# Kernel optimization log

Hardware: AMD Instinct MI355X
Metric: run time of the kernel (lower is better)

The kernel has to match this reference:

```python
import jax, jax.numpy as jnp
import numpy as np

N = 500_000      # num nodes
E = 8_000_000    # num edges (before self-loops)
F_IN, H, C = 16, 8, 2


def setup_inputs() -> dict:
    key = jax.random.key(0)
    k = jax.random.split(key, 6)
    x = jax.random.normal(k[0], (N, F_IN), dtype=jnp.float32)
    edge_index = jax.random.randint(k[1], (2, E), 0, N, dtype=jnp.int32)
    # Glorot-style init like PyG GCNConv
    W1 = jax.random.normal(k[2], (F_IN, H), dtype=jnp.float32) * (1.0 / np.sqrt(F_IN))
    b1 = jnp.zeros((H,), dtype=jnp.float32)
    W2 = jax.random.normal(k[3], (H, C), dtype=jnp.float32) * (1.0 / np.sqrt(H))
    b2 = jnp.zeros((C,), dtype=jnp.float32)
    return {"x": x, "W1": W1, "b1": b1, "W2": W2, "b2": b2, "edge_index": edge_index}


def reference(x, W1, b1, W2, b2, edge_index):
    # GCNConv: out = D^{-1/2} (A + I) D^{-1/2} X W + b   (PyG semantics)
    row, col = edge_index[0], edge_index[1]           # messages flow row -> col
    loop = jnp.arange(N, dtype=row.dtype)
    row = jnp.concatenate([row, loop])                # add self-loops
    col = jnp.concatenate([col, loop])
    deg = jax.ops.segment_sum(jnp.ones_like(col, dtype=x.dtype), col, num_segments=N)
    dinv = jnp.where(deg > 0, jax.lax.rsqrt(deg), jnp.zeros_like(deg))
    norm = dinv[row] * dinv[col]                      # [E+N]

    def propagate(h):  # h: [N, d] -> normalized scatter-add aggregation
        msg = h[row] * norm[:, None]                  # gather + scale, [E+N, d]
        return jax.ops.segment_sum(msg, col, num_segments=N)

    h = jax.nn.relu(propagate(x @ W1) + b1)           # [N, 8]
    out = propagate(h @ W2) + b2                      # [N, 2]
    return jax.nn.log_softmax(out, axis=1)
```

## Files before the change

kernel.cpp:

```cpp
#include <hip/hip_runtime.h>

#define TPB 256
#define NBLK_EDGE 512
#define CHUNKE 16384
#define BIN_SHIFT 9
#define BIN_SIZE 512
#define MAXK 1024
#define ROW_BITS 19
#define ROW_MASK ((1u << ROW_BITS) - 1)
#define Q_SHIFT 17
#define NKEY 2048
#define CAP 12288

typedef _Float16 half8  __attribute__((ext_vector_type(8)));
typedef _Float16 half2v __attribute__((ext_vector_type(2)));

__device__ __forceinline__ int wave_scan_incl(int v, int lane) {
#pragma unroll
    for (int d = 1; d < 64; d <<= 1) {
        int u = __shfl_up(v, d, 64);
        if (lane >= d) v += u;
    }
    return v;
}

__device__ __forceinline__ int block_excl_scan_1024(int v, int tid, int* wsum) {
    int lane = tid & 63, wv = tid >> 6;
    int incl = wave_scan_incl(v, lane);
    if (lane == 63) wsum[wv] = incl;
    __syncthreads();
    if (tid < 16) {
        int w = wsum[tid];
#pragma unroll
        for (int d = 1; d < 16; d <<= 1) {
            int u = __shfl_up(w, d, 16);
            if (tid >= d) w += u;
        }
        wsum[tid] = w;
    }
    __syncthreads();
    return incl - v + (wv ? wsum[wv - 1] : 0);
}

__global__ void __launch_bounds__(1024) k_hist(
        const int* __restrict__ col, int E, int chunk,
        int* __restrict__ cntB, int* __restrict__ cntT) {
    __shared__ int lh[MAXK];
    int blk = blockIdx.x, tid = threadIdx.x;
    lh[tid] = 0;
    __syncthreads();
    int s = blk * chunk, e_ = min(s + chunk, E);
    for (int e = s + tid; e < e_; e += 1024)
        atomicAdd(&lh[col[e] >> BIN_SHIFT], 1);
    __syncthreads();
    int v = lh[tid];
    cntB[(size_t)blk * MAXK + tid] = v;
    cntT[(size_t)tid * NBLK_EDGE + blk] = v;
}

__global__ void k_colscan(int* __restrict__ cntT, int* __restrict__ ghist) {
    __shared__ int part[256];
    int b = blockIdx.x, tid = threadIdx.x;
    size_t base = (size_t)b * NBLK_EDGE;
    int t2 = tid * 2;
    int c0 = cntT[base + t2], c1 = cntT[base + t2 + 1];
    int sum = c0 + c1;
    part[tid] = sum;
    __syncthreads();
    for (int off = 1; off < 256; off <<= 1) {
        int v = (tid >= off) ? part[tid - off] : 0;
        __syncthreads();
        part[tid] += v;
        __syncthreads();
    }
    int excl = part[tid] - sum;
    cntT[base + t2]     = excl;
    cntT[base + t2 + 1] = excl + c0;
    if (tid == 255) ghist[b] = part[255];
}

__global__ void __launch_bounds__(1024) k_scan(
        const int* __restrict__ ghist, int K, int* __restrict__ binBase,
        int* __restrict__ scratchCur) {
    __shared__ int wsum[16];
    int tid = threadIdx.x;
    if (tid == 0) *scratchCur = 0;
    int val = (tid < K) ? ghist[tid] : 0;
    int excl = block_excl_scan_1024(val, tid, wsum);
    binBase[tid] = excl;
    if (tid == K - 1) binBase[K] = excl + val;
}

__global__ void __launch_bounds__(1024) k_reorder(
        const int* __restrict__ row, const int* __restrict__ col,
        int E, int chunk,
        const int* __restrict__ binBase, const int* __restrict__ cntB,
        const int* __restrict__ cntT, unsigned* __restrict__ packed) {
    __shared__ unsigned sorted[CHUNKE];
    __shared__ unsigned short sbin[CHUNKE];
    __shared__ int lcur[MAXK], lbase[MAXK], gbase[MAXK];
    __shared__ int wsum[16];
    int blk = blockIdx.x, tid = threadIdx.x;
    int s = blk * chunk, e_ = min(s + chunk, E), len = e_ - s;
    size_t bb = (size_t)blk * MAXK;
    int c0 = cntB[bb + tid];
    int excl = block_excl_scan_1024(c0, tid, wsum);
    lbase[tid] = excl;
    lcur[tid] = excl;
    gbase[tid] = binBase[tid] + cntT[(size_t)tid * NBLK_EDGE + blk];
    __syncthreads();
    for (int i = tid; i < len; i += blockDim.x) {
        int cc = col[s + i];
        int b = cc >> BIN_SHIFT;
        int slot = atomicAdd(&lcur[b], 1);
        sorted[slot] = ((unsigned)(cc & (BIN_SIZE - 1)) << ROW_BITS) | (unsigned)row[s + i];
        sbin[slot] = (unsigned short)b;
    }
    __syncthreads();
    for (int i = tid; i < len; i += blockDim.x) {
        int b = sbin[i];
        packed[gbase[b] + (i - lbase[b])] = sorted[i];
    }
}

__global__ void __launch_bounds__(1024) k_binsort(
        unsigned* __restrict__ packed, const int* __restrict__ binBase,
        unsigned* __restrict__ scratch, int* __restrict__ scratchCur,
        const float* __restrict__ x, const float* __restrict__ W1,
        half8* __restrict__ g0, int* __restrict__ keyptr, int N, int E, int K) {
    __shared__ unsigned buf2[CAP];
    __shared__ int cnt[NKEY], cur[NKEY];
    __shared__ float w1s[128];
    __shared__ int wsum[16];
    __shared__ int sbShared;
    int tid = threadIdx.x;
    int bin = blockIdx.x;
    int s = binBase[bin], t = binBase[bin + 1];
    int len = t - s;
    bool fast = (len <= CAP);
    cnt[tid] = 0;
    cnt[tid + 1024] = 0;
    if (tid < 128) w1s[tid] = W1[tid];
    if (!fast && tid == 0) sbShared = atomicAdd(scratchCur, len);
    __syncthreads();
    for (int i = tid; i < len; i += 1024) {
        unsigned v = packed[s + i];
        int k = (int)((v >> ROW_BITS) << 2) | (int)((v & ROW_MASK) >> Q_SHIFT);
        atomicAdd(&cnt[k], 1);
    }
    __syncthreads();
    int t2 = tid * 2;
    int c0 = cnt[t2], c1 = cnt[t2 + 1];
    int excl = block_excl_scan_1024(c0 + c1, tid, wsum);
    cur[t2] = excl;
    cur[t2 + 1] = excl + c0;
    int base = bin << BIN_SHIFT;
    if (base + (t2 >> 2) < N) keyptr[((size_t)bin << 11) + t2] = s + excl;
    if (base + ((t2 + 1) >> 2) < N) keyptr[((size_t)bin << 11) + t2 + 1] = s + excl + c0;
    float di = 0.0f;
    int node = base + tid;
    if (tid < BIN_SIZE && node < N) {
        int deg = cnt[4 * tid] + cnt[4 * tid + 1] + cnt[4 * tid + 2] + cnt[4 * tid + 3];
        di = rsqrtf((float)(deg + 1));
    }
    if (bin == K - 1 && tid == 0) keyptr[(size_t)4 * N] = E;
    __syncthreads();
    if (fast) {
        for (int i = tid; i < len; i += 1024) {
            unsigned v = packed[s + i];
            int k = (int)((v >> ROW_BITS) << 2) | (int)((v & ROW_MASK) >> Q_SHIFT);
            int slot = atomicAdd(&cur[k], 1);
            buf2[slot] = v;
        }
        __syncthreads();
        for (int i = tid; i < len; i += 1024) packed[s + i] = buf2[i];
    } else {
        unsigned* stg = scratch + sbShared;
        for (int i = tid; i < len; i += 1024) stg[i] = packed[s + i];
        __threadfence();
        __syncthreads();
        for (int i = tid; i < len; i += 1024) {
            unsigned v = stg[i];
            int k = (int)((v >> ROW_BITS) << 2) | (int)((v & ROW_MASK) >> Q_SHIFT);
            int slot = atomicAdd(&cur[k], 1);
            packed[s + slot] = v;
        }
    }
    if (tid < BIN_SIZE && node < N) {
        const float4* xv = (const float4*)(x + (size_t)node * 16);
        float h[8];
#pragma unroll
        for (int j = 0; j < 8; ++j) h[j] = 0.0f;
#pragma unroll
        for (int kk = 0; kk < 4; ++kk) {
            float4 a = xv[kk];
            int kb = kk * 4;
#pragma unroll
            for (int j = 0; j < 8; ++j)
                h[j] += a.x * w1s[kb * 8 + j] + a.y * w1s[(kb + 1) * 8 + j]
                      + a.z * w1s[(kb + 2) * 8 + j] + a.w * w1s[(kb + 3) * 8 + j];
        }
        half8 g;
#pragma unroll
        for (int j = 0; j < 8; ++j) g[j] = (_Float16)(di * h[j]);
        g0[node] = g;
    }
}

__global__ void __launch_bounds__(TPB) k_gather1(
        const unsigned* __restrict__ packed, const int* __restrict__ keyptr,
        const half8* __restrict__ g0, const float* __restrict__ b1,
        const float* __restrict__ W2, half2v* __restrict__ g1, int N) {
    int i = blockIdx.x * blockDim.x + threadIdx.x;
    bool act = (i < N);
    int kp0 = 0, kp1 = 0, kp2 = 0, kp3 = 0, kp4 = 0;
    if (act) {
        int4 k4 = ((const int4*)keyptr)[i];
        kp0 = k4.x; kp1 = k4.y; kp2 = k4.z; kp3 = k4.w;
        kp4 = keyptr[4 * i + 4];
    }
    float acc[8];
#pragma unroll
    for (int j = 0; j < 8; ++j) acc[j] = 0.0f;
#pragma unroll
    for (int q = 0; q < 4; ++q) {
        int e = (q == 0) ? kp0 : (q == 1) ? kp1 : (q == 2) ? kp2 : kp3;
        int t = (q == 0) ? kp1 : (q == 1) ? kp2 : (q == 2) ? kp3 : kp4;
        if (act) {
            for (; e + 4 <= t; e += 4) {
                unsigned p0 = packed[e], p1 = packed[e + 1],
                         p2 = packed[e + 2], p3 = packed[e + 3];
                half8 v0 = g0[p0 & ROW_MASK];
                half8 v1 = g0[p1 & ROW_MASK];
                half8 v2 = g0[p2 & ROW_MASK];
                half8 v3 = g0[p3 & ROW_MASK];
#pragma unroll
                for (int j = 0; j < 8; ++j)
                    acc[j] += (float)v0[j] + (float)v1[j] + (float)v2[j] + (float)v3[j];
            }
            for (; e < t; ++e) {
                half8 v = g0[packed[e] & ROW_MASK];
#pragma unroll
                for (int j = 0; j < 8; ++j) acc[j] += (float)v[j];
            }
        }
        __syncthreads();
    }
    if (act) {
        half8 self = g0[i];
        float di = rsqrtf((float)(kp4 - kp0 + 1));
        float o0 = 0.0f, o1 = 0.0f;
#pragma unroll
        for (int j = 0; j < 8; ++j) {
            float hj = fmaxf(di * (acc[j] + (float)self[j]) + b1[j], 0.0f);
            o0 += hj * W2[j * 2 + 0];
            o1 += hj * W2[j * 2 + 1];
        }
        half2v g;
        g.x = (_Float16)(di * o0);
        g.y = (_Float16)(di * o1);
        g1[i] = g;
    }
}

__global__ void __launch_bounds__(TPB) k_gather2(
        const unsigned* __restrict__ packed, const int* __restrict__ keyptr,
        const half2v* __restrict__ g1, const float* __restrict__ b2,
        float* __restrict__ out, int N) {
    int i = blockIdx.x * blockDim.x + threadIdx.x;
    if (i >= N) return;
    int s = keyptr[4 * i], t = keyptr[4 * i + 4];
    half2v sg = g1[i];
    float a0 = (float)sg.x, a1 = (float)sg.y;
    int e = s;
    for (; e + 4 <= t; e += 4) {
        unsigned p0 = packed[e], p1 = packed[e + 1], p2 = packed[e + 2], p3 = packed[e + 3];
        half2v v0 = g1[p0 & ROW_MASK];
        half2v v1 = g1[p1 & ROW_MASK];
        half2v v2 = g1[p2 & ROW_MASK];
        half2v v3 = g1[p3 & ROW_MASK];
        a0 += (float)v0.x + (float)v1.x + (float)v2.x + (float)v3.x;
        a1 += (float)v0.y + (float)v1.y + (float)v2.y + (float)v3.y;
    }
    for (; e < t; ++e) {
        half2v v = g1[packed[e] & ROW_MASK];
        a0 += (float)v.x;
        a1 += (float)v.y;
    }
    float di = rsqrtf((float)(t - s + 1));
    float o0 = di * a0 + b2[0];
    float o1 = di * a1 + b2[1];
    float m = fmaxf(o0, o1);
    float lse = m + logf(expf(o0 - m) + expf(o1 - m));
    ((float2*)out)[i] = make_float2(o0 - lse, o1 - lse);
}

extern "C" void kernel_launch(void* const* d_in, const int* in_sizes, int n_in,
                              void* d_out, int out_size, void* d_ws, size_t ws_size,
                              hipStream_t stream) {
    const float* x  = (const float*)d_in[0];
    const float* W1 = (const float*)d_in[1];
    const float* b1 = (const float*)d_in[2];
    const float* W2 = (const float*)d_in[3];
    const float* b2 = (const float*)d_in[4];
    const int*   ei = (const int*)d_in[5];

    const int N = in_sizes[0] / 16;
    const int E = in_sizes[5] / 2;
    const int* row = ei;
    const int* col = ei + E;
    const int K = (N + BIN_SIZE - 1) >> BIN_SHIFT;

    float* ws   = (float*)d_ws;
    half8* g0   = (half8*)ws;
    half2v* g1  = (half2v*)(ws + (size_t)4 * N);
    unsigned* scratch = (unsigned*)(ws + (size_t)5 * N);
    int* keyptr = (int*)(ws + (size_t)13 * N);
    int*   meta = (int*)(ws + (size_t)17 * N + 8);
    int* ghist      = meta;
    int* binBase    = meta + MAXK;
    int* scratchCur = meta + 2 * MAXK + 16;
    unsigned* packed = (unsigned*)(meta + 3 * MAXK);
    int* cntB = (int*)(packed + E);
    int* cntT = cntB + (size_t)MAXK * NBLK_EDGE;

    float* out = (float*)d_out;

    const int gN = (N + TPB - 1) / TPB;
    const int chunk = (E + NBLK_EDGE - 1) / NBLK_EDGE;

    k_hist   <<<NBLK_EDGE, 1024, 0, stream>>>(col, E, chunk, cntB, cntT);
    k_colscan<<<K, 256, 0, stream>>>(cntT, ghist);
    k_scan   <<<1, MAXK, 0, stream>>>(ghist, K, binBase, scratchCur);
    k_reorder<<<NBLK_EDGE, 1024, 0, stream>>>(row, col, E, chunk,
                                              binBase, cntB, cntT, packed);
    k_binsort<<<K, 1024, 0, stream>>>(packed, binBase, scratch, scratchCur,
                                      x, W1, g0, keyptr, N, E, K);
    k_gather1<<<gN, TPB, 0, stream>>>(packed, keyptr, g0, b1, W2, g1, N);
    k_gather2<<<gN, TPB, 0, stream>>>(packed, keyptr, g1, b2, out, N);
}
```

Measured before the change: 351.2 us.

## Use 16-lane groups per node in gathers and drop quadrant subkey sort

The two gather kernels now assign a 16-lane group to each destination node, striding over its edges and reducing with xor shuffles, instead of one thread walking every edge of a node. The bin sort now keys only on the destination column, dropping the row-quadrant subkey, so keyptr shrinks to N+1 offsets and the workspace layout is compacted. The intent is to remove load imbalance and serial edge loops in the gathers and to make the packed index reads coalesced. The trade-off is losing the row-ordered locality the quadrant subsort gave within each node's edge list, and most lanes sit idle once a node has fewer than 16 edges.

```diff
diff --git a/kernel.cpp b/kernel.cpp
--- a/kernel.cpp
+++ b/kernel.cpp
@@ -8,9 +8,8 @@
 #define MAXK 1024
 #define ROW_BITS 19
 #define ROW_MASK ((1u << ROW_BITS) - 1)
-#define Q_SHIFT 17
-#define NKEY 2048
 #define CAP 12288
+#define GV_TPB 512
 
 typedef _Float16 half8  __attribute__((ext_vector_type(8)));
 typedef _Float16 half2v __attribute__((ext_vector_type(2)));
@@ -129,7 +128,7 @@
         const float* __restrict__ x, const float* __restrict__ W1,
         half8* __restrict__ g0, int* __restrict__ keyptr, int N, int E, int K) {
     __shared__ unsigned buf2[CAP];
-    __shared__ int cnt[NKEY], cur[NKEY];
+    __shared__ int cnt[BIN_SIZE], cur[BIN_SIZE];
     __shared__ float w1s[128];
     __shared__ int wsum[16];
     __shared__ int sbShared;
@@ -138,38 +137,31 @@
     int s = binBase[bin], t = binBase[bin + 1];
     int len = t - s;
     bool fast = (len <= CAP);
-    cnt[tid] = 0;
-    cnt[tid + 1024] = 0;
+    if (tid < BIN_SIZE) cnt[tid] = 0;
     if (tid < 128) w1s[tid] = W1[tid];
     if (!fast && tid == 0) sbShared = atomicAdd(scratchCur, len);
     __syncthreads();
     for (int i = tid; i < len; i += 1024) {
         unsigned v = packed[s + i];
-        int k = (int)((v >> ROW_BITS) << 2) | (int)((v & ROW_MASK) >> Q_SHIFT);
-        atomicAdd(&cnt[k], 1);
-    }
-    __syncthreads();
-    int t2 = tid * 2;
-    int c0 = cnt[t2], c1 = cnt[t2 + 1];
-    int excl = block_excl_scan_1024(c0 + c1, tid, wsum);
-    cur[t2] = excl;
-    cur[t2 + 1] = excl + c0;
+        atomicAdd(&cnt[v >> ROW_BITS], 1);
+    }
+    __syncthreads();
+    int c0 = (tid < BIN_SIZE) ? cnt[tid] : 0;
+    int excl = block_excl_scan_1024(c0, tid, wsum);
     int base = bin << BIN_SHIFT;
-    if (base + (t2 >> 2) < N) keyptr[((size_t)bin << 11) + t2] = s + excl;
-    if (base + ((t2 + 1) >> 2) < N) keyptr[((size_t)bin << 11) + t2 + 1] = s + excl + c0;
+    int node = base + tid;
     float di = 0.0f;
-    int node = base + tid;
-    if (tid < BIN_SIZE && node < N) {
-        int deg = cnt[4 * tid] + cnt[4 * tid + 1] + cnt[4 * tid + 2] + cnt[4 * tid + 3];
-        di = rsqrtf((float)(deg + 1));
-    }
-    if (bin == K - 1 && tid == 0) keyptr[(size_t)4 * N] = E;
+    if (tid < BIN_SIZE) {
+        cur[tid] = excl;
+        if (node < N) keyptr[node] = s + excl;
+        di = rsqrtf((float)(c0 + 1));
+    }
+    if (bin == K - 1 && tid == 0) keyptr[N] = E;
     __syncthreads();
     if (fast) {
         for (int i = tid; i < len; i += 1024) {
             unsigned v = packed[s + i];
-            int k = (int)((v >> ROW_BITS) << 2) | (int)((v & ROW_MASK) >> Q_SHIFT);
-            int slot = atomicAdd(&cur[k], 1);
+            int slot = atomicAdd(&cur[v >> ROW_BITS], 1);
             buf2[slot] = v;
         }
         __syncthreads();
@@ -181,8 +173,7 @@
         __syncthreads();
         for (int i = tid; i < len; i += 1024) {
             unsigned v = stg[i];
-            int k = (int)((v >> ROW_BITS) << 2) | (int)((v & ROW_MASK) >> Q_SHIFT);
-            int slot = atomicAdd(&cur[k], 1);
+            int slot = atomicAdd(&cur[v >> ROW_BITS], 1);
             packed[s + slot] = v;
         }
     }
@@ -207,48 +198,30 @@
     }
 }
 
-__global__ void __launch_bounds__(TPB) k_gather1(
+__global__ void __launch_bounds__(GV_TPB) k_gather1(
         const unsigned* __restrict__ packed, const int* __restrict__ keyptr,
         const half8* __restrict__ g0, const float* __restrict__ b1,
         const float* __restrict__ W2, half2v* __restrict__ g1, int N) {
-    int i = blockIdx.x * blockDim.x + threadIdx.x;
-    bool act = (i < N);
-    int kp0 = 0, kp1 = 0, kp2 = 0, kp3 = 0, kp4 = 0;
-    if (act) {
-        int4 k4 = ((const int4*)keyptr)[i];
-        kp0 = k4.x; kp1 = k4.y; kp2 = k4.z; kp3 = k4.w;
-        kp4 = keyptr[4 * i + 4];
-    }
+    int tid = threadIdx.x;
+    int lane16 = tid & 15;
+    int node = blockIdx.x * (GV_TPB / 16) + (tid >> 4);
+    if (node >= N) return;
+    int s = keyptr[node], t = keyptr[node + 1];
     float acc[8];
 #pragma unroll
     for (int j = 0; j < 8; ++j) acc[j] = 0.0f;
-#pragma unroll
-    for (int q = 0; q < 4; ++q) {
-        int e = (q == 0) ? kp0 : (q == 1) ? kp1 : (q == 2) ? kp2 : kp3;
-        int t = (q == 0) ? kp1 : (q == 1) ? kp2 : (q == 2) ? kp3 : kp4;
-        if (act) {
-            for (; e + 4 <= t; e += 4) {
-                unsigned p0 = packed[e], p1 = packed[e + 1],
-                         p2 = packed[e + 2], p3 = packed[e + 3];
-                half8 v0 = g0[p0 & ROW_MASK];
-                half8 v1 = g0[p1 & ROW_MASK];
-                half8 v2 = g0[p2 & ROW_MASK];
-                half8 v3 = g0[p3 & ROW_MASK];
-#pragma unroll
-                for (int j = 0; j < 8; ++j)
-                    acc[j] += (float)v0[j] + (float)v1[j] + (float)v2[j] + (float)v3[j];
-            }
-            for (; e < t; ++e) {
-                half8 v = g0[packed[e] & ROW_MASK];
-#pragma unroll
-                for (int j = 0; j < 8; ++j) acc[j] += (float)v[j];
-            }
-        }
-        __syncthreads();
-    }
-    if (act) {
-        half8 self = g0[i];
-        float di = rsqrtf((float)(kp4 - kp0 + 1));
+    for (int e = s + lane16; e < t; e += 16) {
+        half8 v = g0[packed[e] & ROW_MASK];
+#pragma unroll
+        for (int j = 0; j < 8; ++j) acc[j] += (float)v[j];
+    }
+#pragma unroll
+    for (int d = 1; d < 16; d <<= 1)
+#pragma unroll
+        for (int j = 0; j < 8; ++j) acc[j] += __shfl_xor(acc[j], d, 64);
+    if (lane16 == 0) {
+        half8 self = g0[node];
+        float di = rsqrtf((float)(t - s + 1));
         float o0 = 0.0f, o1 = 0.0f;
 #pragma unroll
         for (int j = 0; j < 8; ++j) {
@@ -259,40 +232,39 @@
         half2v g;
         g.x = (_Float16)(di * o0);
         g.y = (_Float16)(di * o1);
-        g1[i] = g;
-    }
-}
-
-__global__ void __launch_bounds__(TPB) k_gather2(
+        g1[node] = g;
+    }
+}
+
+__global__ void __launch_bounds__(GV_TPB) k_gather2(
         const unsigned* __restrict__ packed, const int* __restrict__ keyptr,
         const half2v* __restrict__ g1, const float* __restrict__ b2,
         float* __restrict__ out, int N) {
-    int i = blockIdx.x * blockDim.x + threadIdx.x;
-    if (i >= N) return;
-    int s = keyptr[4 * i], t = keyptr[4 * i + 4];
-    half2v sg = g1[i];
-    float a0 = (float)sg.x, a1 = (float)sg.y;
-    int e = s;
-    for (; e + 4 <= t; e += 4) {
-        unsigned p0 = packed[e], p1 = packed[e + 1], p2 = packed[e + 2], p3 = packed[e + 3];
-        half2v v0 = g1[p0 & ROW_MASK];
-        half2v v1 = g1[p1 & ROW_MASK];
-        half2v v2 = g1[p2 & ROW_MASK];
-        half2v v3 = g1[p3 & ROW_MASK];
-        a0 += (float)v0.x + (float)v1.x + (float)v2.x + (float)v3.x;
-        a1 += (float)v0.y + (float)v1.y + (float)v2.y + (float)v3.y;
-    }
-    for (; e < t; ++e) {
+    int tid = threadIdx.x;
+    int lane16 = tid & 15;
+    int node = blockIdx.x * (GV_TPB / 16) + (tid >> 4);
+    if (node >= N) return;
+    int s = keyptr[node], t = keyptr[node + 1];
+    float a0 = 0.0f, a1 = 0.0f;
+    for (int e = s + lane16; e < t; e += 16) {
         half2v v = g1[packed[e] & ROW_MASK];
         a0 += (float)v.x;
         a1 += (float)v.y;
     }
-    float di = rsqrtf((float)(t - s + 1));
-    float o0 = di * a0 + b2[0];
-    float o1 = di * a1 + b2[1];
-    float m = fmaxf(o0, o1);
-    float lse = m + logf(expf(o0 - m) + expf(o1 - m));
-    ((float2*)out)[i] = make_float2(o0 - lse, o1 - lse);
+#pragma unroll
+    for (int d = 1; d < 16; d <<= 1) {
+        a0 += __shfl_xor(a0, d, 64);
+        a1 += __shfl_xor(a1, d, 64);
+    }
+    if (lane16 == 0) {
+        half2v self = g1[node];
+        float di = rsqrtf((float)(t - s + 1));
+        float o0 = di * (a0 + (float)self.x) + b2[0];
+        float o1 = di * (a1 + (float)self.y) + b2[1];
+        float m = fmaxf(o0, o1);
+        float lse = m + logf(expf(o0 - m) + expf(o1 - m));
+        ((float2*)out)[node] = make_float2(o0 - lse, o1 - lse);
+    }
 }
 
 extern "C" void kernel_launch(void* const* d_in, const int* in_sizes, int n_in,
@@ -316,7 +288,7 @@
     half2v* g1  = (half2v*)(ws + (size_t)4 * N);
     unsigned* scratch = (unsigned*)(ws + (size_t)5 * N);
     int* keyptr = (int*)(ws + (size_t)13 * N);
-    int*   meta = (int*)(ws + (size_t)17 * N + 8);
+    int*   meta = (int*)(ws + (size_t)15 * N);
     int* ghist      = meta;
     int* binBase    = meta + MAXK;
     int* scratchCur = meta + 2 * MAXK + 16;
@@ -326,7 +298,7 @@
 
     float* out = (float*)d_out;
 
-    const int gN = (N + TPB - 1) / TPB;
+    const int gV = (N + (GV_TPB / 16) - 1) / (GV_TPB / 16);
     const int chunk = (E + NBLK_EDGE - 1) / NBLK_EDGE;
 
     k_hist   <<<NBLK_EDGE, 1024, 0, stream>>>(col, E, chunk, cntB, cntT);
@@ -336,6 +308,6 @@
                                               binBase, cntB, cntT, packed);
     k_binsort<<<K, 1024, 0, stream>>>(packed, binBase, scratch, scratchCur,
                                       x, W1, g0, keyptr, N, E, K);
-    k_gather1<<<gN, TPB, 0, stream>>>(packed, keyptr, g0, b1, W2, g1, N);
-    k_gather2<<<gN, TPB, 0, stream>>>(packed, keyptr, g1, b2, out, N);
-}
+    k_gather1<<<gV, GV_TPB, 0, stream>>>(packed, keyptr, g0, b1, W2, g1, N);
+    k_gather2<<<gV, GV_TPB, 0, stream>>>(packed, keyptr, g1, b2, out, N);
+}
```

After: 349.2 us. Within noise of the previous version (-0.6%).
